# Kernel optimization log

Measured on AMD Instinct MI355X. Metric: run time of the kernel, lower is better.

Reference implementation:

```python
import jax, jax.numpy as jnp
import numpy as np

ALPHA = 1.5  # entmax alpha (EntmaxBisect default behavior, exponent 1/(alpha-1)=2)
N_ITER = 50  # EntmaxBisect default number of bisection iterations


def entmax_bisect(x, alpha=ALPHA, n_iter=N_ITER):
    """Entmax via bisection along the last axis (Peters & Martins), matching
    the torch entmax.EntmaxBisect forward (with ensure_sum_one=True)."""
    d = x.shape[-1]
    xs = x * (alpha - 1.0)
    max_val = jnp.max(xs, axis=-1, keepdims=True)
    tau_lo = max_val - 1.0
    tau_hi = max_val - (1.0 / d) ** (alpha - 1.0)

    inv_am1 = 1.0 / (alpha - 1.0)  # = 2.0 for alpha=1.5

    def p(tau):
        return jnp.maximum(xs - tau, 0.0) ** inv_am1

    f_lo = jnp.sum(p(tau_lo), axis=-1, keepdims=True) - 1.0
    dm0 = tau_hi - tau_lo

    def body(i, carry):
        tau_lo, dm = carry
        dm = dm * 0.5
        tau_m = tau_lo + dm
        f_m = jnp.sum(p(tau_m), axis=-1, keepdims=True) - 1.0
        tau_lo = jnp.where(f_m * f_lo >= 0, tau_m, tau_lo)
        return (tau_lo, dm)

    tau_lo, dm = jax.lax.fori_loop(0, n_iter, body, (tau_lo, dm0))
    p_m = p(tau_lo + dm)
    return p_m / jnp.sum(p_m, axis=-1, keepdims=True)


def setup_inputs() -> dict:
    key = jax.random.key(0)
    k1, k2, k3, k4 = jax.random.split(key, 4)
    bsz, nfield, nemb = 2048, 128, 128
    nhead, nhid, d_k = 8, 64, 64

    def xavier(k, shape, gain=1.414):
        fan_in, fan_out = shape[-2], shape[-1]
        std = gain * np.sqrt(2.0 / (fan_in + fan_out))
        return jax.random.normal(k, shape, dtype=jnp.float32) * std

    return {
        "x": jax.random.normal(k1, (bsz, nfield, nemb), dtype=jnp.float32),
        "bilinear_w": xavier(k2, (nhead, nemb, d_k)),
        "query": xavier(k3, (nhead, nhid, d_k)),
        "values": xavier(k4, (nhead, nhid, nfield)),
    }


def reference(x, bilinear_w, query, values):
    # x: [b, f, x(=nemb)]; bilinear_w: [k, x, y(=d_k)]; query: [k, o(=nhid), y]
    d_k = bilinear_w.shape[-1]
    scale = d_k ** (-0.5)
    # einsum('bfx,kxy,koy->bkof') split into two contractions
    kx = jnp.einsum('bfx,kxy->bkfy', x, bilinear_w)            # [b,k,f,y]
    att_gates = jnp.einsum('bkfy,koy->bkof', kx, query) * scale  # [b,k,o,f]
    sparse_gates = entmax_bisect(att_gates)
    return sparse_gates * values[None]  # einsum('bkof,kof->bkof')
```

## Files before the change

### kernel.cpp

```cpp
#include <hip/hip_runtime.h>
#include <hip/hip_bf16.h>


using half8_t  = __attribute__((ext_vector_type(8))) _Float16;
using half4_t  = __attribute__((ext_vector_type(4))) _Float16;
using fp16x2   = __attribute__((ext_vector_type(2))) __fp16;
using floatx4  = __attribute__((ext_vector_type(4))) float;

#define NBIS 8

#if defined(__has_builtin)
#if __has_builtin(__builtin_amdgcn_fdot2)
#define HAS_FDOT2 1
#endif
#endif
#ifndef HAS_FDOT2
#define HAS_FDOT2 0
#endif

__device__ __forceinline__ float frcp(float x) {
#if __has_builtin(__builtin_amdgcn_rcpf)
    return __builtin_amdgcn_rcpf(x);
#else
    return 1.0f / x;
#endif
}

__global__ __launch_bounds__(256) void w2_kernel(const float* __restrict__ bw,
                                                 const float* __restrict__ qm,
                                                 _Float16* __restrict__ W2h) {
    const int k  = blockIdx.x >> 3;
    const int og = blockIdx.x & 7;
    __shared__ float Lbw[128 * 65];
    __shared__ float Lq[8 * 64];
    const int t = threadIdx.x;

    const float* bwk = bw + k * 8192;
    #pragma unroll
    for (int i2 = 0; i2 < 8; ++i2) {
        int i = t + i2 * 256;
        float4 v = ((const float4*)bwk)[i];
        int xx = (i * 4) >> 6, y = (i * 4) & 63;
        float* dst = &Lbw[xx * 65 + y];
        dst[0] = v.x; dst[1] = v.y; dst[2] = v.z; dst[3] = v.w;
    }
    const float* qk = qm + k * 4096 + og * 8 * 64;
    if (t < 128) ((float4*)Lq)[t] = ((const float4*)qk)[t];
    __syncthreads();

    #pragma unroll
    for (int i = 0; i < 4; ++i) {
        int ox = i * 256 + t;
        int o = ox >> 7, x = ox & 127;
        const float* brow = &Lbw[x * 65];
        const float* qrow = &Lq[o * 64];
        float acc = 0.f;
        #pragma unroll
        for (int y = 0; y < 64; ++y) acc = fmaf(brow[y], qrow[y], acc);
        W2h[(k * 64 + og * 8 + o) * 128 + x] = (_Float16)(acc * 0.0625f);
    }
}

__global__ __launch_bounds__(256) void xh_kernel(const float* __restrict__ xg,
                                                 _Float16* __restrict__ xh) {
    const size_t n4 = (size_t)2048 * 128 * 32;
    const size_t stride = (size_t)gridDim.x * 256;
    for (size_t i = (size_t)blockIdx.x * 256 + threadIdx.x; i < n4; i += stride) {
        float4 v = ((const float4*)xg)[i];
        half4_t h;
        h[0] = (_Float16)v.x; h[1] = (_Float16)v.y;
        h[2] = (_Float16)v.z; h[3] = (_Float16)v.w;
        ((half4_t*)xh)[i] = h;
    }
}

template<bool PRE>
__global__ __launch_bounds__(256, 6) void satt_kernel(
        const float* __restrict__ xg, const _Float16* __restrict__ Xh,
        const _Float16* __restrict__ W2h,
        const float* __restrict__ values, float* __restrict__ out) {
    const int bid = blockIdx.x;
    const int k = (bid & 511) >> 6;
    const int b = ((bid >> 9) << 6) | (bid & 63);
    const int t = threadIdx.x;
    const int w = t >> 6, l = t & 63;
    const int q = l >> 4, c16 = l & 15;
    const int o = w * 16 + c16;

    half8_t bfrag[4];
    const _Float16* w2row = W2h + ((k * 64 + o) << 7);
    #pragma unroll
    for (int kk = 0; kk < 4; ++kk)
        bfrag[kk] = *(const half8_t*)(w2row + kk * 32 + q * 8);

    floatx4 acc[8];
    #pragma unroll
    for (int mt = 0; mt < 8; ++mt) acc[mt] = (floatx4){0.f, 0.f, 0.f, 0.f};

    if (PRE) {
        const _Float16* xb = Xh + (size_t)b * 16384;
        #pragma unroll
        for (int kk = 0; kk < 4; ++kk) {
            #pragma unroll
            for (int mt = 0; mt < 8; ++mt) {
                half8_t a = *(const half8_t*)(xb + (mt * 16 + c16) * 128 + kk * 32 + q * 8);
                acc[mt] = __builtin_amdgcn_mfma_f32_16x16x32_f16(a, bfrag[kk], acc[mt], 0, 0, 0);
            }
        }
    } else {
        const float* xb = xg + (size_t)b * 16384;
        #pragma unroll
        for (int kk = 0; kk < 4; ++kk) {
            #pragma unroll
            for (int mt = 0; mt < 8; ++mt) {
                const float4* p = (const float4*)(xb + (mt * 16 + c16) * 128 + kk * 32 + q * 8);
                float4 v0 = p[0], v1 = p[1];
                half8_t a;
                a[0] = (_Float16)v0.x; a[1] = (_Float16)v0.y;
                a[2] = (_Float16)v0.z; a[3] = (_Float16)v0.w;
                a[4] = (_Float16)v1.x; a[5] = (_Float16)v1.y;
                a[6] = (_Float16)v1.z; a[7] = (_Float16)v1.w;
                acc[mt] = __builtin_amdgcn_mfma_f32_16x16x32_f16(a, bfrag[kk], acc[mt], 0, 0, 0);
            }
        }
    }

    float zz[32];
    #pragma unroll
    for (int mt = 0; mt < 8; ++mt) {
        zz[4 * mt + 0] = acc[mt][0]; zz[4 * mt + 1] = acc[mt][1];
        zz[4 * mt + 2] = acc[mt][2]; zz[4 * mt + 3] = acc[mt][3];
    }
    float m0 = zz[0], m1 = zz[1], m2 = zz[2], m3 = zz[3];
    #pragma unroll
    for (int j = 4; j < 32; j += 4) {
        m0 = fmaxf(m0, zz[j + 0]); m1 = fmaxf(m1, zz[j + 1]);
        m2 = fmaxf(m2, zz[j + 2]); m3 = fmaxf(m3, zz[j + 3]);
    }
    float m = fmaxf(fmaxf(m0, m1), fmaxf(m2, m3));
    m = fmaxf(m, __shfl_xor(m, 16));
    m = fmaxf(m, __shfl_xor(m, 32));

    float tau = m - 1.0f;
    float dm  = 0.9116116523516816f;

#if HAS_FDOT2
    fp16x2 zh[16];
    #pragma unroll
    for (int j = 0; j < 16; ++j)
        zh[j] = __builtin_amdgcn_cvt_pkrtz(zz[2 * j], zz[2 * j + 1]);
    const fp16x2 hzero = { (__fp16)0.f, (__fp16)0.f };
    const fp16x2 hone  = { (__fp16)1.f, (__fp16)1.f };

    #pragma unroll
    for (int it = 0; it < NBIS; ++it) {
        dm *= 0.5f;
        float tm = tau + dm;
        fp16x2 t2 = __builtin_amdgcn_cvt_pkrtz(tm, tm);
        float sa = 0.f, sb = 0.f;
        #pragma unroll
        for (int j = 0; j < 16; j += 2) {
            fp16x2 d0 = __builtin_elementwise_max(zh[j]     - t2, hzero);
            fp16x2 d1 = __builtin_elementwise_max(zh[j + 1] - t2, hzero);
            sa = __builtin_amdgcn_fdot2(d0, d0, sa, false);
            sb = __builtin_amdgcn_fdot2(d1, d1, sb, false);
        }
        float sm = sa + sb;
        sm += __shfl_xor(sm, 16); sm += __shfl_xor(sm, 32);
        tau = (sm >= 1.0f) ? tm : tau;
    }
    #pragma unroll
    for (int it = 0; it < 2; ++it) {
        fp16x2 t2 = __builtin_amdgcn_cvt_pkrtz(tau, tau);
        float s2a = 0.f, s2b = 0.f, s1a = 0.f, s1b = 0.f;
        #pragma unroll
        for (int j = 0; j < 16; j += 2) {
            fp16x2 d0 = __builtin_elementwise_max(zh[j]     - t2, hzero);
            fp16x2 d1 = __builtin_elementwise_max(zh[j + 1] - t2, hzero);
            s2a = __builtin_amdgcn_fdot2(d0, d0, s2a, false);
            s2b = __builtin_amdgcn_fdot2(d1, d1, s2b, false);
            s1a = __builtin_amdgcn_fdot2(d0, hone, s1a, false);
            s1b = __builtin_amdgcn_fdot2(d1, hone, s1b, false);
        }
        float s2 = s2a + s2b, s1 = s1a + s1b;
        s2 += __shfl_xor(s2, 16); s2 += __shfl_xor(s2, 32);
        s1 += __shfl_xor(s1, 16); s1 += __shfl_xor(s1, 32);
        tau += (s2 - 1.0f) * frcp(fmaxf(s1 + s1, 1e-6f));
    }
#else
    #pragma unroll
    for (int it = 0; it < NBIS + 4; ++it) {
        dm *= 0.5f;
        float tm = tau + dm;
        float sa = 0.f, sb = 0.f;
        #pragma unroll
        for (int j = 0; j < 32; j += 2) {
            float d0 = fmaxf(zz[j] - tm, 0.f);
            float d1 = fmaxf(zz[j + 1] - tm, 0.f);
            sa = fmaf(d0, d0, sa); sb = fmaf(d1, d1, sb);
        }
        float sm = sa + sb;
        sm += __shfl_xor(sm, 16); sm += __shfl_xor(sm, 32);
        tau = (sm >= 1.0f) ? tm : tau;
    }
    {
        float s2a = 0.f, s2b = 0.f, s1a = 0.f, s1b = 0.f;
        #pragma unroll
        for (int j = 0; j < 32; j += 2) {
            float d0 = fmaxf(zz[j] - tau, 0.f);
            float d1 = fmaxf(zz[j + 1] - tau, 0.f);
            s2a = fmaf(d0, d0, s2a); s2b = fmaf(d1, d1, s2b);
            s1a += d0; s1b += d1;
        }
        float s2 = s2a + s2b, s1 = s1a + s1b;
        s2 += __shfl_xor(s2, 16); s2 += __shfl_xor(s2, 32);
        s1 += __shfl_xor(s1, 16); s1 += __shfl_xor(s1, 32);
        tau += (s2 - 1.0f) * frcp(fmaxf(s1 + s1, 1e-6f));
    }
#endif
    {
        float s2a = 0.f, s2b = 0.f, s1a = 0.f, s1b = 0.f;
        #pragma unroll
        for (int j = 0; j < 32; j += 2) {
            float d0 = fmaxf(zz[j] - tau, 0.f);
            float d1 = fmaxf(zz[j + 1] - tau, 0.f);
            s2a = fmaf(d0, d0, s2a); s2b = fmaf(d1, d1, s2b);
            s1a += d0; s1b += d1;
        }
        float s2 = s2a + s2b, s1 = s1a + s1b;
        s2 += __shfl_xor(s2, 16); s2 += __shfl_xor(s2, 32);
        s1 += __shfl_xor(s1, 16); s1 += __shfl_xor(s1, 32);
        tau += (s2 - 1.0f) * frcp(fmaxf(s1 + s1, 1e-6f));
    }

    float ps0 = 0.f, ps1 = 0.f;
    #pragma unroll
    for (int j = 0; j < 32; j += 2) {
        float d0 = fmaxf(zz[j] - tau, 0.f);
        float d1 = fmaxf(zz[j + 1] - tau, 0.f);
        float p0 = d0 * d0, p1 = d1 * d1;
        zz[j] = p0; zz[j + 1] = p1;
        ps0 += p0; ps1 += p1;
    }
    float ps = ps0 + ps1;
    ps += __shfl_xor(ps, 16); ps += __shfl_xor(ps, 32);
    const float inv = 1.0f / ps;

    const float* vrow = values + ((k * 64 + o) << 7) + q * 4;
    float* orow = out + ((((size_t)b * 8 + k) * 64 + o) << 7) + q * 4;
    #pragma unroll
    for (int mt = 0; mt < 8; ++mt) {
        floatx4 vv = *(const floatx4*)(vrow + mt * 16);
        floatx4 g;
        g[0] = zz[4 * mt + 0] * inv * vv[0];
        g[1] = zz[4 * mt + 1] * inv * vv[1];
        g[2] = zz[4 * mt + 2] * inv * vv[2];
        g[3] = zz[4 * mt + 3] * inv * vv[3];
        *(floatx4*)(orow + mt * 16) = g;
    }
}

extern "C" void kernel_launch(void* const* d_in, const int* in_sizes, int n_in,
                              void* d_out, int out_size, void* d_ws, size_t ws_size,
                              hipStream_t stream) {
    const float* xg     = (const float*)d_in[0];
    const float* bw     = (const float*)d_in[1];
    const float* qm     = (const float*)d_in[2];
    const float* values = (const float*)d_in[3];
    float* out = (float*)d_out;
    _Float16* W2h = (_Float16*)d_ws;
    _Float16* Xh  = (_Float16*)((char*)d_ws + 131072);

    const size_t need = 131072 + (size_t)2048 * 128 * 128 * 2;

    w2_kernel<<<64, 256, 0, stream>>>(bw, qm, W2h);
    if (ws_size >= need) {
        xh_kernel<<<8192, 256, 0, stream>>>(xg, Xh);
        satt_kernel<true><<<16384, 256, 0, stream>>>(xg, Xh, W2h, values, out);
    } else {
        satt_kernel<false><<<16384, 256, 0, stream>>>(xg, Xh, W2h, values, out);
    }
}
```

Measured before the change: 906.6 us.

## Stage per-batch x tile in LDS as fp16 and loop over heads in-block

The separate fp32-to-fp16 conversion kernel and its workspace round trip are removed. Each block now handles one batch element: it loads x once, converts it to fp16 into padded shared memory, and loops over all 8 heads reusing that tile, prefetching the next head's W2 fragments. This avoids re-reading x from global memory once per head and drops one kernel launch. In exchange the grid shrinks from 16384 to 2048 blocks with about 34 KB of LDS each, and the launch bound changes from 6 to 4 waves, which may lower occupancy and latency hiding.

```diff
diff --git a/kernel.cpp b/kernel.cpp
--- a/kernel.cpp
+++ b/kernel.cpp
@@ -61,202 +61,191 @@
     }
 }
 
-__global__ __launch_bounds__(256) void xh_kernel(const float* __restrict__ xg,
-                                                 _Float16* __restrict__ xh) {
-    const size_t n4 = (size_t)2048 * 128 * 32;
-    const size_t stride = (size_t)gridDim.x * 256;
-    for (size_t i = (size_t)blockIdx.x * 256 + threadIdx.x; i < n4; i += stride) {
-        float4 v = ((const float4*)xg)[i];
+__global__ __launch_bounds__(256, 4) void satt_kernel(
+        const float* __restrict__ xg, const _Float16* __restrict__ W2h,
+        const float* __restrict__ values, float* __restrict__ out) {
+    const int b = blockIdx.x;
+    const int t = threadIdx.x;
+    const int qtr = t >> 6, l = t & 63;
+    const int q = l >> 4, c16 = l & 15;
+    const int o = qtr * 16 + c16;
+
+    __shared__ _Float16 Ash[128 * 136];
+
+    const float* xb = xg + (size_t)b * 16384;
+    #pragma unroll
+    for (int j = 0; j < 16; ++j) {
+        int c = t + 256 * j;
+        int f = c >> 5, x0 = (c & 31) * 4;
+        float4 v = ((const float4*)xb)[c];
         half4_t h;
         h[0] = (_Float16)v.x; h[1] = (_Float16)v.y;
         h[2] = (_Float16)v.z; h[3] = (_Float16)v.w;
-        ((half4_t*)xh)[i] = h;
-    }
-}
-
-template<bool PRE>
-__global__ __launch_bounds__(256, 6) void satt_kernel(
-        const float* __restrict__ xg, const _Float16* __restrict__ Xh,
-        const _Float16* __restrict__ W2h,
-        const float* __restrict__ values, float* __restrict__ out) {
-    const int bid = blockIdx.x;
-    const int k = (bid & 511) >> 6;
-    const int b = ((bid >> 9) << 6) | (bid & 63);
-    const int t = threadIdx.x;
-    const int w = t >> 6, l = t & 63;
-    const int q = l >> 4, c16 = l & 15;
-    const int o = w * 16 + c16;
-
-    half8_t bfrag[4];
-    const _Float16* w2row = W2h + ((k * 64 + o) << 7);
+        *(half4_t*)(&Ash[f * 136 + x0]) = h;
+    }
+    __syncthreads();
+
+    const _Float16* w2o = W2h + (o << 7) + q * 8;
+    half8_t bcur[4], bnxt[4];
     #pragma unroll
     for (int kk = 0; kk < 4; ++kk)
-        bfrag[kk] = *(const half8_t*)(w2row + kk * 32 + q * 8);
-
-    floatx4 acc[8];
-    #pragma unroll
-    for (int mt = 0; mt < 8; ++mt) acc[mt] = (floatx4){0.f, 0.f, 0.f, 0.f};
-
-    if (PRE) {
-        const _Float16* xb = Xh + (size_t)b * 16384;
+        bcur[kk] = *(const half8_t*)(w2o + kk * 32);
+
+    #pragma unroll 2
+    for (int k = 0; k < 8; ++k) {
+        const _Float16* w2n = w2o + (((k + 1) & 7) << 13);
+        #pragma unroll
+        for (int kk = 0; kk < 4; ++kk)
+            bnxt[kk] = *(const half8_t*)(w2n + kk * 32);
+
+        floatx4 acc[8];
+        #pragma unroll
+        for (int mt = 0; mt < 8; ++mt) acc[mt] = (floatx4){0.f, 0.f, 0.f, 0.f};
         #pragma unroll
         for (int kk = 0; kk < 4; ++kk) {
             #pragma unroll
             for (int mt = 0; mt < 8; ++mt) {
-                half8_t a = *(const half8_t*)(xb + (mt * 16 + c16) * 128 + kk * 32 + q * 8);
-                acc[mt] = __builtin_amdgcn_mfma_f32_16x16x32_f16(a, bfrag[kk], acc[mt], 0, 0, 0);
-            }
-        }
-    } else {
-        const float* xb = xg + (size_t)b * 16384;
-        #pragma unroll
-        for (int kk = 0; kk < 4; ++kk) {
-            #pragma unroll
-            for (int mt = 0; mt < 8; ++mt) {
-                const float4* p = (const float4*)(xb + (mt * 16 + c16) * 128 + kk * 32 + q * 8);
-                float4 v0 = p[0], v1 = p[1];
-                half8_t a;
-                a[0] = (_Float16)v0.x; a[1] = (_Float16)v0.y;
-                a[2] = (_Float16)v0.z; a[3] = (_Float16)v0.w;
-                a[4] = (_Float16)v1.x; a[5] = (_Float16)v1.y;
-                a[6] = (_Float16)v1.z; a[7] = (_Float16)v1.w;
-                acc[mt] = __builtin_amdgcn_mfma_f32_16x16x32_f16(a, bfrag[kk], acc[mt], 0, 0, 0);
-            }
-        }
-    }
-
-    float zz[32];
-    #pragma unroll
-    for (int mt = 0; mt < 8; ++mt) {
-        zz[4 * mt + 0] = acc[mt][0]; zz[4 * mt + 1] = acc[mt][1];
-        zz[4 * mt + 2] = acc[mt][2]; zz[4 * mt + 3] = acc[mt][3];
-    }
-    float m0 = zz[0], m1 = zz[1], m2 = zz[2], m3 = zz[3];
-    #pragma unroll
-    for (int j = 4; j < 32; j += 4) {
-        m0 = fmaxf(m0, zz[j + 0]); m1 = fmaxf(m1, zz[j + 1]);
-        m2 = fmaxf(m2, zz[j + 2]); m3 = fmaxf(m3, zz[j + 3]);
-    }
-    float m = fmaxf(fmaxf(m0, m1), fmaxf(m2, m3));
-    m = fmaxf(m, __shfl_xor(m, 16));
-    m = fmaxf(m, __shfl_xor(m, 32));
-
-    float tau = m - 1.0f;
-    float dm  = 0.9116116523516816f;
+                half8_t a = *(const half8_t*)(&Ash[(mt * 16 + c16) * 136 + kk * 32 + q * 8]);
+                acc[mt] = __builtin_amdgcn_mfma_f32_16x16x32_f16(a, bcur[kk], acc[mt], 0, 0, 0);
+            }
+        }
+
+        float zz[32];
+        #pragma unroll
+        for (int mt = 0; mt < 8; ++mt) {
+            zz[4 * mt + 0] = acc[mt][0]; zz[4 * mt + 1] = acc[mt][1];
+            zz[4 * mt + 2] = acc[mt][2]; zz[4 * mt + 3] = acc[mt][3];
+        }
+        float m0 = zz[0], m1 = zz[1], m2 = zz[2], m3 = zz[3];
+        #pragma unroll
+        for (int j = 4; j < 32; j += 4) {
+            m0 = fmaxf(m0, zz[j + 0]); m1 = fmaxf(m1, zz[j + 1]);
+            m2 = fmaxf(m2, zz[j + 2]); m3 = fmaxf(m3, zz[j + 3]);
+        }
+        float m = fmaxf(fmaxf(m0, m1), fmaxf(m2, m3));
+        m = fmaxf(m, __shfl_xor(m, 16));
+        m = fmaxf(m, __shfl_xor(m, 32));
+
+        float tau = m - 1.0f;
+        float dm  = 0.9116116523516816f;
 
 #if HAS_FDOT2
-    fp16x2 zh[16];
-    #pragma unroll
-    for (int j = 0; j < 16; ++j)
-        zh[j] = __builtin_amdgcn_cvt_pkrtz(zz[2 * j], zz[2 * j + 1]);
-    const fp16x2 hzero = { (__fp16)0.f, (__fp16)0.f };
-    const fp16x2 hone  = { (__fp16)1.f, (__fp16)1.f };
-
-    #pragma unroll
-    for (int it = 0; it < NBIS; ++it) {
-        dm *= 0.5f;
-        float tm = tau + dm;
-        fp16x2 t2 = __builtin_amdgcn_cvt_pkrtz(tm, tm);
-        float sa = 0.f, sb = 0.f;
-        #pragma unroll
-        for (int j = 0; j < 16; j += 2) {
-            fp16x2 d0 = __builtin_elementwise_max(zh[j]     - t2, hzero);
-            fp16x2 d1 = __builtin_elementwise_max(zh[j + 1] - t2, hzero);
-            sa = __builtin_amdgcn_fdot2(d0, d0, sa, false);
-            sb = __builtin_amdgcn_fdot2(d1, d1, sb, false);
-        }
-        float sm = sa + sb;
-        sm += __shfl_xor(sm, 16); sm += __shfl_xor(sm, 32);
-        tau = (sm >= 1.0f) ? tm : tau;
-    }
-    #pragma unroll
-    for (int it = 0; it < 2; ++it) {
-        fp16x2 t2 = __builtin_amdgcn_cvt_pkrtz(tau, tau);
-        float s2a = 0.f, s2b = 0.f, s1a = 0.f, s1b = 0.f;
-        #pragma unroll
-        for (int j = 0; j < 16; j += 2) {
-            fp16x2 d0 = __builtin_elementwise_max(zh[j]     - t2, hzero);
-            fp16x2 d1 = __builtin_elementwise_max(zh[j + 1] - t2, hzero);
-            s2a = __builtin_amdgcn_fdot2(d0, d0, s2a, false);
-            s2b = __builtin_amdgcn_fdot2(d1, d1, s2b, false);
-            s1a = __builtin_amdgcn_fdot2(d0, hone, s1a, false);
-            s1b = __builtin_amdgcn_fdot2(d1, hone, s1b, false);
-        }
-        float s2 = s2a + s2b, s1 = s1a + s1b;
-        s2 += __shfl_xor(s2, 16); s2 += __shfl_xor(s2, 32);
-        s1 += __shfl_xor(s1, 16); s1 += __shfl_xor(s1, 32);
-        tau += (s2 - 1.0f) * frcp(fmaxf(s1 + s1, 1e-6f));
-    }
+        fp16x2 zh[16];
+        #pragma unroll
+        for (int j = 0; j < 16; ++j)
+            zh[j] = __builtin_amdgcn_cvt_pkrtz(zz[2 * j], zz[2 * j + 1]);
+        const fp16x2 hzero = { (__fp16)0.f, (__fp16)0.f };
+        const fp16x2 hone  = { (__fp16)1.f, (__fp16)1.f };
+
+        #pragma unroll
+        for (int it = 0; it < NBIS; ++it) {
+            dm *= 0.5f;
+            float tm = tau + dm;
+            fp16x2 t2 = __builtin_amdgcn_cvt_pkrtz(tm, tm);
+            float sa = 0.f, sb = 0.f;
+            #pragma unroll
+            for (int j = 0; j < 16; j += 2) {
+                fp16x2 d0 = __builtin_elementwise_max(zh[j]     - t2, hzero);
+                fp16x2 d1 = __builtin_elementwise_max(zh[j + 1] - t2, hzero);
+                sa = __builtin_amdgcn_fdot2(d0, d0, sa, false);
+                sb = __builtin_amdgcn_fdot2(d1, d1, sb, false);
+            }
+            float sm = sa + sb;
+            sm += __shfl_xor(sm, 16); sm += __shfl_xor(sm, 32);
+            tau = (sm >= 1.0f) ? tm : tau;
+        }
+        #pragma unroll
+        for (int it = 0; it < 2; ++it) {
+            fp16x2 t2 = __builtin_amdgcn_cvt_pkrtz(tau, tau);
+            float s2a = 0.f, s2b = 0.f, s1a = 0.f, s1b = 0.f;
+            #pragma unroll
+            for (int j = 0; j < 16; j += 2) {
+                fp16x2 d0 = __builtin_elementwise_max(zh[j]     - t2, hzero);
+                fp16x2 d1 = __builtin_elementwise_max(zh[j + 1] - t2, hzero);
+                s2a = __builtin_amdgcn_fdot2(d0, d0, s2a, false);
+                s2b = __builtin_amdgcn_fdot2(d1, d1, s2b, false);
+                s1a = __builtin_amdgcn_fdot2(d0, hone, s1a, false);
+                s1b = __builtin_amdgcn_fdot2(d1, hone, s1b, false);
+            }
+            float s2 = s2a + s2b, s1 = s1a + s1b;
+            s2 += __shfl_xor(s2, 16); s2 += __shfl_xor(s2, 32);
+            s1 += __shfl_xor(s1, 16); s1 += __shfl_xor(s1, 32);
+            tau += (s2 - 1.0f) * frcp(fmaxf(s1 + s1, 1e-6f));
+        }
 #else
-    #pragma unroll
-    for (int it = 0; it < NBIS + 4; ++it) {
-        dm *= 0.5f;
-        float tm = tau + dm;
-        float sa = 0.f, sb = 0.f;
-        #pragma unroll
-        for (int j = 0; j < 32; j += 2) {
-            float d0 = fmaxf(zz[j] - tm, 0.f);
-            float d1 = fmaxf(zz[j + 1] - tm, 0.f);
-            sa = fmaf(d0, d0, sa); sb = fmaf(d1, d1, sb);
-        }
-        float sm = sa + sb;
-        sm += __shfl_xor(sm, 16); sm += __shfl_xor(sm, 32);
-        tau = (sm >= 1.0f) ? tm : tau;
-    }
-    {
-        float s2a = 0.f, s2b = 0.f, s1a = 0.f, s1b = 0.f;
+        #pragma unroll
+        for (int it = 0; it < NBIS + 4; ++it) {
+            dm *= 0.5f;
+            float tm = tau + dm;
+            float sa = 0.f, sb = 0.f;
+            #pragma unroll
+            for (int j = 0; j < 32; j += 2) {
+                float d0 = fmaxf(zz[j] - tm, 0.f);
+                float d1 = fmaxf(zz[j + 1] - tm, 0.f);
+                sa = fmaf(d0, d0, sa); sb = fmaf(d1, d1, sb);
+            }
+            float sm = sa + sb;
+            sm += __shfl_xor(sm, 16); sm += __shfl_xor(sm, 32);
+            tau = (sm >= 1.0f) ? tm : tau;
+        }
+        {
+            float s2a = 0.f, s2b = 0.f, s1a = 0.f, s1b = 0.f;
+            #pragma unroll
+            for (int j = 0; j < 32; j += 2) {
+                float d0 = fmaxf(zz[j] - tau, 0.f);
+                float d1 = fmaxf(zz[j + 1] - tau, 0.f);
+                s2a = fmaf(d0, d0, s2a); s2b = fmaf(d1, d1, s2b);
+                s1a += d0; s1b += d1;
+            }
+            float s2 = s2a + s2b, s1 = s1a + s1b;
+            s2 += __shfl_xor(s2, 16); s2 += __shfl_xor(s2, 32);
+            s1 += __shfl_xor(s1, 16); s1 += __shfl_xor(s1, 32);
+            tau += (s2 - 1.0f) * frcp(fmaxf(s1 + s1, 1e-6f));
+        }
+#endif
+        {
+            float s2a = 0.f, s2b = 0.f, s1a = 0.f, s1b = 0.f;
+            #pragma unroll
+            for (int j = 0; j < 32; j += 2) {
+                float d0 = fmaxf(zz[j] - tau, 0.f);
+                float d1 = fmaxf(zz[j + 1] - tau, 0.f);
+                s2a = fmaf(d0, d0, s2a); s2b = fmaf(d1, d1, s2b);
+                s1a += d0; s1b += d1;
+            }
+            float s2 = s2a + s2b, s1 = s1a + s1b;
+            s2 += __shfl_xor(s2, 16); s2 += __shfl_xor(s2, 32);
+            s1 += __shfl_xor(s1, 16); s1 += __shfl_xor(s1, 32);
+            tau += (s2 - 1.0f) * frcp(fmaxf(s1 + s1, 1e-6f));
+        }
+
+        float ps0 = 0.f, ps1 = 0.f;
         #pragma unroll
         for (int j = 0; j < 32; j += 2) {
             float d0 = fmaxf(zz[j] - tau, 0.f);
             float d1 = fmaxf(zz[j + 1] - tau, 0.f);
-            s2a = fmaf(d0, d0, s2a); s2b = fmaf(d1, d1, s2b);
-            s1a += d0; s1b += d1;
-        }
-        float s2 = s2a + s2b, s1 = s1a + s1b;
-        s2 += __shfl_xor(s2, 16); s2 += __shfl_xor(s2, 32);
-        s1 += __shfl_xor(s1, 16); s1 += __shfl_xor(s1, 32);
-        tau += (s2 - 1.0f) * frcp(fmaxf(s1 + s1, 1e-6f));
-    }
-#endif
-    {
-        float s2a = 0.f, s2b = 0.f, s1a = 0.f, s1b = 0.f;
-        #pragma unroll
-        for (int j = 0; j < 32; j += 2) {
-            float d0 = fmaxf(zz[j] - tau, 0.f);
-            float d1 = fmaxf(zz[j + 1] - tau, 0.f);
-            s2a = fmaf(d0, d0, s2a); s2b = fmaf(d1, d1, s2b);
-            s1a += d0; s1b += d1;
-        }
-        float s2 = s2a + s2b, s1 = s1a + s1b;
-        s2 += __shfl_xor(s2, 16); s2 += __shfl_xor(s2, 32);
-        s1 += __shfl_xor(s1, 16); s1 += __shfl_xor(s1, 32);
-        tau += (s2 - 1.0f) * frcp(fmaxf(s1 + s1, 1e-6f));
-    }
-
-    float ps0 = 0.f, ps1 = 0.f;
-    #pragma unroll
-    for (int j = 0; j < 32; j += 2) {
-        float d0 = fmaxf(zz[j] - tau, 0.f);
-        float d1 = fmaxf(zz[j + 1] - tau, 0.f);
-        float p0 = d0 * d0, p1 = d1 * d1;
-        zz[j] = p0; zz[j + 1] = p1;
-        ps0 += p0; ps1 += p1;
-    }
-    float ps = ps0 + ps1;
-    ps += __shfl_xor(ps, 16); ps += __shfl_xor(ps, 32);
-    const float inv = 1.0f / ps;
-
-    const float* vrow = values + ((k * 64 + o) << 7) + q * 4;
-    float* orow = out + ((((size_t)b * 8 + k) * 64 + o) << 7) + q * 4;
-    #pragma unroll
-    for (int mt = 0; mt < 8; ++mt) {
-        floatx4 vv = *(const floatx4*)(vrow + mt * 16);
-        floatx4 g;
-        g[0] = zz[4 * mt + 0] * inv * vv[0];
-        g[1] = zz[4 * mt + 1] * inv * vv[1];
-        g[2] = zz[4 * mt + 2] * inv * vv[2];
-        g[3] = zz[4 * mt + 3] * inv * vv[3];
-        *(floatx4*)(orow + mt * 16) = g;
+            float p0 = d0 * d0, p1 = d1 * d1;
+            zz[j] = p0; zz[j + 1] = p1;
+            ps0 += p0; ps1 += p1;
+        }
+        float ps = ps0 + ps1;
+        ps += __shfl_xor(ps, 16); ps += __shfl_xor(ps, 32);
+        const float inv = 1.0f / ps;
+
+        const float* vrow = values + ((k * 64 + o) << 7) + q * 4;
+        float* orow = out + ((((size_t)b * 8 + k) * 64 + o) << 7) + q * 4;
+        #pragma unroll
+        for (int mt = 0; mt < 8; ++mt) {
+            floatx4 vv = *(const floatx4*)(vrow + mt * 16);
+            floatx4 g;
+            g[0] = zz[4 * mt + 0] * inv * vv[0];
+            g[1] = zz[4 * mt + 1] * inv * vv[1];
+            g[2] = zz[4 * mt + 2] * inv * vv[2];
+            g[3] = zz[4 * mt + 3] * inv * vv[3];
+            *(floatx4*)(orow + mt * 16) = g;
+        }
+
+        #pragma unroll
+        for (int kk = 0; kk < 4; ++kk) bcur[kk] = bnxt[kk];
     }
 }
 
@@ -269,15 +258,7 @@
     const float* values = (const float*)d_in[3];
     float* out = (float*)d_out;
     _Float16* W2h = (_Float16*)d_ws;
-    _Float16* Xh  = (_Float16*)((char*)d_ws + 131072);
-
-    const size_t need = 131072 + (size_t)2048 * 128 * 128 * 2;
 
     w2_kernel<<<64, 256, 0, stream>>>(bw, qm, W2h);
-    if (ws_size >= need) {
-        xh_kernel<<<8192, 256, 0, stream>>>(xg, Xh);
-        satt_kernel<true><<<16384, 256, 0, stream>>>(xg, Xh, W2h, values, out);
-    } else {
-        satt_kernel<false><<<16384, 256, 0, stream>>>(xg, Xh, W2h, values, out);
-    }
-}
+    satt_kernel<<<2048, 256, 0, stream>>>(xg, W2h, values, out);
+}
```

Result: slower. 925.7 us (+2.1%).
